# Optimization experiments

Hardware: AMD Instinct MI355X
Metric: run time of the kernel (lower is better)

Reference implementation:

```python
import jax, jax.numpy as jnp
import numpy as np

# B3-spline 5-tap kernel [1/16, 1/4, 3/8, 1/4, 1/16]
W5 = (1.0/16.0, 1.0/4.0, 3.0/8.0, 1.0/4.0, 1.0/16.0)
LEVEL = 3  # J


def _b3_conv1d(x, axis, dilation):
    """Dilated 5-tap B3-spline conv along `axis` with reflect padding (same size)."""
    p = 2 * dilation  # torch uses padding=2**(i+1) = 2*dilation
    pad_cfg = [(p, p) if a == axis else (0, 0) for a in range(x.ndim)]
    xp = jnp.pad(x, pad_cfg, mode='reflect')
    L = x.shape[axis]
    out = W5[0] * jax.lax.slice_in_dim(xp, 0, L, axis=axis)
    for k in range(1, 5):
        out = out + W5[k] * jax.lax.slice_in_dim(xp, k * dilation, k * dilation + L, axis=axis)
    return out


def setup_inputs() -> dict:
    key = jax.random.key(0)
    x = jax.random.normal(key, (16, 1024, 1024), dtype=jnp.float32)
    return {"x": x}


def reference(x):
    # x: (B, H, W). Returns (B, J+1, H, W) = [w_1, ..., w_J, c_J].
    y = x
    outs = []
    for i in range(LEVEL):
        d = 2 ** i
        prev = y
        for axis in (1, 2):  # separable 1D convs along H then W
            y = _b3_conv1d(y, axis, d)
        outs.append(prev - y)  # wavelet coefficients w_{i+1}
    outs.append(y)  # residual c_J
    return jnp.stack(outs, axis=1)
```

## Files before the change

### kernel.cpp

```cpp
#include <hip/hip_runtime.h>
#include <stdint.h>


typedef float     f4v __attribute__((ext_vector_type(4)));
typedef _Float16  h2v __attribute__((ext_vector_type(2)));

constexpr int TB  = 256;
constexpr int VH  = 14;
constexpr int XR  = 92;
constexpr int XCP = 93;
constexpr int U1P = 69;
constexpr int U2P = 77;
constexpr int HW  = 1024 * 1024;

__device__ constexpr float K13f[13] = {
    1.f/256, 4.f/256, 10.f/256, 20.f/256, 31.f/256, 40.f/256, 44.f/256,
    40.f/256, 31.f/256, 20.f/256, 10.f/256, 4.f/256, 1.f/256};
__device__ constexpr float K29f[29] = {
    1.f/4096,   4.f/4096,  10.f/4096,  20.f/4096,  35.f/4096,  56.f/4096,
    84.f/4096, 120.f/4096, 161.f/4096, 204.f/4096, 246.f/4096, 284.f/4096,
    315.f/4096, 336.f/4096, 344.f/4096, 336.f/4096, 315.f/4096, 284.f/4096,
    246.f/4096, 204.f/4096, 161.f/4096, 120.f/4096,  84.f/4096,  56.f/4096,
    35.f/4096,  20.f/4096,  10.f/4096,   4.f/4096,   1.f/4096};

__device__ __forceinline__ int refl(int i) {
    return i < 0 ? -i : (i >= 1024 ? 2046 - i : i);
}
__device__ __forceinline__ uint32_t b32(h2v v) { return __builtin_bit_cast(uint32_t, v); }
__device__ __forceinline__ h2v hb(uint32_t v)  { return __builtin_bit_cast(h2v, v); }
__device__ __forceinline__ uint32_t pkrtz(float a, float b) {
    return __builtin_bit_cast(uint32_t, __builtin_amdgcn_cvt_pkrtz(a, b));
}
__device__ __forceinline__ h2v algn(h2v hi, h2v lo) {
    return hb(__builtin_amdgcn_alignbit(b32(hi), b32(lo), 16));
}
__device__ __forceinline__ h2v hsplat(float f) {
    const _Float16 h = (_Float16)f;
    return h2v{h, h};
}
__device__ __forceinline__ f4v tof4(h2v a, h2v b) {
    return f4v{(float)a[0], (float)a[1], (float)b[0], (float)b[1]};
}

__global__ __launch_bounds__(TB)
void uwt3_kernel(const float* __restrict__ x, float* __restrict__ out)
{
    __shared__ uint2 xsw[24 * XCP];
    __shared__ uint2 u1b[16 * U1P];
    __shared__ uint2 u2b[16 * U2P];

    const int tid = threadIdx.x;

    const int flat = blockIdx.x;
    const int swz  = (flat & 7) * 512 + (flat >> 3);
    const int bxi = swz & 15;
    const int byi = (swz >> 4) & 15;
    const int bz  = swz >> 8;
    const int bx = bxi * 64;
    const int by = byi * 64;

    const float* xp = x + (size_t)bz * HW;
    float* op = out + (size_t)bz * 4 * HW;

    for (int e = tid; e < XR * 24; e += TB) {
        const int r = e / 24, m = e - r * 24;
        const int gr = refl(by - VH + r);
        const int gc0 = bx - 16 + 4 * m;
        f4v v;
        if (gc0 >= 0 && gc0 <= 1020) {
            v = *(const f4v*)(xp + (size_t)gr * 1024 + gc0);
        } else {
#pragma unroll
            for (int q = 0; q < 4; ++q) v[q] = xp[(size_t)gr * 1024 + refl(gc0 + q)];
        }
        xsw[m * XCP + r] = uint2{pkrtz(v[0], v[1]), pkrtz(v[2], v[3])};
    }
    __syncthreads();

    const h2v W0 = hsplat(0.0625f), W1 = hsplat(0.25f), W2 = hsplat(0.375f);

    for (int t = tid; t < XR * 4; t += TB) {
        const int gi = t & 3;
        const int rp = t >> 2;
        const uint2* base = xsw + (4 * gi) * XCP + rp;
        h2v H[24];
#pragma unroll
        for (int j = 0; j < 12; ++j) {
            const uint2 w = base[j * XCP];
            H[2*j]   = hb(w.x);
            H[2*j+1] = hb(w.y);
        }
        {
            h2v roll = algn(H[2], H[1]);
#pragma unroll
            for (int p = 1; p <= 20; ++p) {
                const h2v a1 = roll;
                const h2v a3 = algn(H[p+2], H[p+1]);
                roll = a3;
                H[p] = W0 * (H[p] + H[p+2]) + W1 * (a1 + a3) + W2 * H[p+1];
            }
        }
        if (rp >= 12 && rp < 80) {
            uint2* d = u1b + (4 * gi) * U1P + (rp - 12);
#pragma unroll
            for (int j = 0; j < 4; ++j)
                d[j * U1P] = uint2{b32(H[7 + 2*j]), b32(H[8 + 2*j])};
        }
#pragma unroll
        for (int p = 1; p <= 16; ++p)
            H[p] = W0 * (H[p] + H[p+4]) + W1 * (H[p+1] + H[p+3]) + W2 * H[p+2];
        if (rp >= 8 && rp < 84) {
            uint2* d = u2b + (4 * gi) * U2P + (rp - 8);
#pragma unroll
            for (int j = 0; j < 4; ++j)
                d[j * U2P] = uint2{b32(H[5 + 2*j]), b32(H[6 + 2*j])};
        }
#pragma unroll
        for (int p = 1; p <= 8; ++p)
            H[p] = W0 * (H[p] + H[p+8]) + W1 * (H[p+2] + H[p+6]) + W2 * H[p+4];
        {
            uint2* d = xsw + (4 * gi) * XCP + rp;
#pragma unroll
            for (int j = 0; j < 4; ++j)
                d[j * XCP] = uint2{b32(H[1 + 2*j]), b32(H[2 + 2*j])};
        }
    }
    __syncthreads();

    const int fc = tid & 15;
    const int r0 = (tid >> 4) * 4;
    const size_t gbase = (size_t)(by + r0) * 1024 + bx + 4 * fc;

    f4v xc[4];
#pragma unroll
    for (int j = 0; j < 4; ++j)
        xc[j] = *(const f4v*)(xp + gbase + (size_t)j * 1024);

    f4v c1f[4];
    {
        const uint2* b1 = u1b + fc * U1P + r0;
        h2v ua[8], ub[8];
#pragma unroll
        for (int i = 0; i < 8; ++i) {
            const uint2 w = b1[i];
            ua[i] = hb(w.x);
            ub[i] = hb(w.y);
        }
#pragma unroll
        for (int j = 0; j < 4; ++j) {
            const h2v s0 = W0 * (ua[j] + ua[j+4]) + W1 * (ua[j+1] + ua[j+3]) + W2 * ua[j+2];
            const h2v s1 = W0 * (ub[j] + ub[j+4]) + W1 * (ub[j+1] + ub[j+3]) + W2 * ub[j+2];
            c1f[j] = tof4(s0, s1);
        }
    }
#pragma unroll
    for (int j = 0; j < 4; ++j)
        __builtin_nontemporal_store(xc[j] - c1f[j],
            (f4v*)(op + 0 * HW + gbase + (size_t)j * 1024));

    f4v c2f[4];
    {
        const uint2* b2 = u2b + fc * U2P + r0;
        h2v A[4][2] = {}, B[4][2] = {};
#pragma unroll
        for (int i = 0; i < 16; ++i) {
            const uint2 w = b2[i];
            const h2v v0 = hb(w.x), v1 = hb(w.y);
#pragma unroll
            for (int j = 0; j < 4; ++j) {
                const int m = i - j;
                if (m >= 0 && m <= 12) {
                    const h2v k = hsplat(K13f[m]);
                    if (i & 1) { B[j][0] += k * v0; B[j][1] += k * v1; }
                    else       { A[j][0] += k * v0; A[j][1] += k * v1; }
                }
            }
        }
#pragma unroll
        for (int j = 0; j < 4; ++j)
            c2f[j] = tof4(A[j][0] + B[j][0], A[j][1] + B[j][1]);
    }
#pragma unroll
    for (int j = 0; j < 4; ++j)
        __builtin_nontemporal_store(c1f[j] - c2f[j],
            (f4v*)(op + 1 * HW + gbase + (size_t)j * 1024));

    f4v c3f[4];
    {
        const uint2* b3 = xsw + fc * XCP + r0;
        h2v A[4][2] = {}, B[4][2] = {};
#pragma unroll
        for (int i = 0; i < 32; ++i) {
            const uint2 w = b3[i];
            const h2v v0 = hb(w.x), v1 = hb(w.y);
#pragma unroll
            for (int j = 0; j < 4; ++j) {
                const int m = i - j;
                if (m >= 0 && m <= 28) {
                    const h2v k = hsplat(K29f[m]);
                    if (i & 1) { B[j][0] += k * v0; B[j][1] += k * v1; }
                    else       { A[j][0] += k * v0; A[j][1] += k * v1; }
                }
            }
        }
#pragma unroll
        for (int j = 0; j < 4; ++j)
            c3f[j] = tof4(A[j][0] + B[j][0], A[j][1] + B[j][1]);
    }
#pragma unroll
    for (int j = 0; j < 4; ++j) {
        __builtin_nontemporal_store(c2f[j] - c3f[j],
            (f4v*)(op + 2 * HW + gbase + (size_t)j * 1024));
        __builtin_nontemporal_store(c3f[j],
            (f4v*)(op + 3 * HW + gbase + (size_t)j * 1024));
    }
}

extern "C" void kernel_launch(void* const* d_in, const int* in_sizes, int n_in,
                              void* d_out, int out_size, void* d_ws, size_t ws_size,
                              hipStream_t stream)
{
    const float* x = (const float*)d_in[0];
    float* out = (float*)d_out;
    uwt3_kernel<<<dim3(4096), dim3(TB), 0, stream>>>(x, out);
}
```

Before: 63.42 us.

## Process two tiles per block and prefetch the second tile's input into registers

Each block now handles two horizontally adjacent 64x64 tiles, halving the grid. The second tile's input halo is loaded into registers while the first tile is filtered and stored, then moved to shared memory. The reflect-edge branch is skipped for tiles not on the image border. This is meant to hide global load latency behind compute. It costs extra registers (NST f4v prefetch buffers, about 36 VGPRs), which may lower occupancy, and the smaller grid may leave fewer blocks to balance across CUs.

Measured after the change: 67.60 us. 6.6% more time.

```diff
diff --git a/kernel.cpp b/kernel.cpp
--- a/kernel.cpp
+++ b/kernel.cpp
@@ -12,6 +12,7 @@
 constexpr int U1P = 69;
 constexpr int U2P = 77;
 constexpr int HW  = 1024 * 1024;
+constexpr int NST = (XR * 24 + TB - 1) / TB;
 
 __device__ constexpr float K13f[13] = {
     1.f/256, 4.f/256, 10.f/256, 20.f/256, 31.f/256, 40.f/256, 44.f/256,
@@ -42,43 +43,29 @@
     return f4v{(float)a[0], (float)a[1], (float)b[0], (float)b[1]};
 }
 
-__global__ __launch_bounds__(TB)
-void uwt3_kernel(const float* __restrict__ x, float* __restrict__ out)
-{
-    __shared__ uint2 xsw[24 * XCP];
-    __shared__ uint2 u1b[16 * U1P];
-    __shared__ uint2 u2b[16 * U2P];
-
-    const int tid = threadIdx.x;
-
-    const int flat = blockIdx.x;
-    const int swz  = (flat & 7) * 512 + (flat >> 3);
-    const int bxi = swz & 15;
-    const int byi = (swz >> 4) & 15;
-    const int bz  = swz >> 8;
-    const int bx = bxi * 64;
-    const int by = byi * 64;
-
-    const float* xp = x + (size_t)bz * HW;
-    float* op = out + (size_t)bz * 4 * HW;
-
-    for (int e = tid; e < XR * 24; e += TB) {
-        const int r = e / 24, m = e - r * 24;
-        const int gr = refl(by - VH + r);
-        const int gc0 = bx - 16 + 4 * m;
-        f4v v;
-        if (gc0 >= 0 && gc0 <= 1020) {
-            v = *(const f4v*)(xp + (size_t)gr * 1024 + gc0);
-        } else {
-#pragma unroll
-            for (int q = 0; q < 4; ++q) v[q] = xp[(size_t)gr * 1024 + refl(gc0 + q)];
-        }
-        xsw[m * XCP + r] = uint2{pkrtz(v[0], v[1]), pkrtz(v[2], v[3])};
-    }
-    __syncthreads();
-
+__device__ __forceinline__ f4v stage_load(const float* __restrict__ xp,
+                                          int e, int bx, int by, bool xedge) {
+    const int r = e / 24, m = e - r * 24;
+    const int gr = refl(by - VH + r);
+    const int gc0 = bx - 16 + 4 * m;
+    f4v v;
+    if (!xedge || (gc0 >= 0 && gc0 <= 1020)) {
+        v = *(const f4v*)(xp + (size_t)gr * 1024 + gc0);
+    } else {
+#pragma unroll
+        for (int q = 0; q < 4; ++q) v[q] = xp[(size_t)gr * 1024 + refl(gc0 + q)];
+    }
+    return v;
+}
+__device__ __forceinline__ void stage_store(uint2* __restrict__ xsw, int e, f4v v) {
+    const int r = e / 24, m = e - r * 24;
+    xsw[m * XCP + r] = uint2{pkrtz(v[0], v[1]), pkrtz(v[2], v[3])};
+}
+
+__device__ __forceinline__ void passA(uint2* __restrict__ xsw,
+                                      uint2* __restrict__ u1b,
+                                      uint2* __restrict__ u2b, int tid) {
     const h2v W0 = hsplat(0.0625f), W1 = hsplat(0.25f), W2 = hsplat(0.375f);
-
     for (int t = tid; t < XR * 4; t += TB) {
         const int gi = t & 3;
         const int rp = t >> 2;
@@ -125,8 +112,15 @@
                 d[j * XCP] = uint2{b32(H[1 + 2*j]), b32(H[2 + 2*j])};
         }
     }
-    __syncthreads();
-
+}
+
+__device__ __forceinline__ void passB(const uint2* __restrict__ xsw,
+                                      const uint2* __restrict__ u1b,
+                                      const uint2* __restrict__ u2b,
+                                      int tid, int bx, int by,
+                                      const float* __restrict__ xp,
+                                      float* __restrict__ op) {
+    const h2v W0 = hsplat(0.0625f), W1 = hsplat(0.25f), W2 = hsplat(0.375f);
     const int fc = tid & 15;
     const int r0 = (tid >> 4) * 4;
     const size_t gbase = (size_t)(by + r0) * 1024 + bx + 4 * fc;
@@ -216,11 +210,67 @@
     }
 }
 
+__global__ __launch_bounds__(TB)
+void uwt3_kernel(const float* __restrict__ x, float* __restrict__ out)
+{
+    __shared__ uint2 xsw[24 * XCP];
+    __shared__ uint2 u1b[16 * U1P];
+    __shared__ uint2 u2b[16 * U2P];
+
+    const int tid = threadIdx.x;
+
+    const int flat = blockIdx.x;
+    const int swz  = (flat & 7) * 256 + (flat >> 3);
+    const int tA = swz * 2;
+    const int tB = tA + 1;
+
+    const int bxiA = tA & 15, byi = (tA >> 4) & 15, bz = tA >> 8;
+    const int bxiB = tB & 15;
+    const int bxA = bxiA * 64, bxB = bxiB * 64;
+    const int by  = byi * 64;
+    const bool edgeA = (bxiA == 0);
+    const bool edgeB = (bxiB == 15);
+
+    const float* xp = x + (size_t)bz * HW;
+    float* op = out + (size_t)bz * 4 * HW;
+
+#pragma unroll
+    for (int it = 0; it < NST; ++it) {
+        const int e = tid + it * TB;
+        if (e < XR * 24) stage_store(xsw, e, stage_load(xp, e, bxA, by, edgeA));
+    }
+    __syncthreads();
+
+    f4v pf[NST];
+#pragma unroll
+    for (int it = 0; it < NST; ++it) {
+        int e = tid + it * TB;
+        if (e >= XR * 24) e = XR * 24 - 1;
+        pf[it] = stage_load(xp, e, bxB, by, edgeB);
+    }
+
+    passA(xsw, u1b, u2b, tid);
+    __syncthreads();
+    passB(xsw, u1b, u2b, tid, bxA, by, xp, op);
+    __syncthreads();
+
+#pragma unroll
+    for (int it = 0; it < NST; ++it) {
+        const int e = tid + it * TB;
+        if (e < XR * 24) stage_store(xsw, e, pf[it]);
+    }
+    __syncthreads();
+
+    passA(xsw, u1b, u2b, tid);
+    __syncthreads();
+    passB(xsw, u1b, u2b, tid, bxB, by, xp, op);
+}
+
 extern "C" void kernel_launch(void* const* d_in, const int* in_sizes, int n_in,
                               void* d_out, int out_size, void* d_ws, size_t ws_size,
                               hipStream_t stream)
 {
     const float* x = (const float*)d_in[0];
     float* out = (float*)d_out;
-    uwt3_kernel<<<dim3(4096), dim3(TB), 0, stream>>>(x, out);
-}
+    uwt3_kernel<<<dim3(2048), dim3(TB), 0, stream>>>(x, out);
+}
```
